# Performance work log

Hardware: AMD Instinct MI355X
Metric: run time of the kernel (lower is better)

The kernel has to match this reference:

```python
import jax, jax.numpy as jnp
import numpy as np

V, H, B, T = 64, 128, 128, 512


def setup_inputs() -> dict:
    key = jax.random.key(0)
    ks = jax.random.split(key, 12)
    s = 0.05
    return {
        "x": jax.random.randint(ks[0], (B, T), 0, V),
        "emb": jax.random.normal(ks[1], (V, H), dtype=jnp.float32) * s,
        "w_ih_f": jax.random.normal(ks[2], (4 * H, H), dtype=jnp.float32) * s,
        "w_hh_f": jax.random.normal(ks[3], (4 * H, H), dtype=jnp.float32) * s,
        "b_ih_f": jax.random.normal(ks[4], (4 * H,), dtype=jnp.float32) * s,
        "b_hh_f": jax.random.normal(ks[5], (4 * H,), dtype=jnp.float32) * s,
        "w_ih_b": jax.random.normal(ks[6], (4 * H, H), dtype=jnp.float32) * s,
        "w_hh_b": jax.random.normal(ks[7], (4 * H, H), dtype=jnp.float32) * s,
        "b_ih_b": jax.random.normal(ks[8], (4 * H,), dtype=jnp.float32) * s,
        "b_hh_b": jax.random.normal(ks[9], (4 * H,), dtype=jnp.float32) * s,
        "fc_w": jax.random.normal(ks[10], (V, 2 * H), dtype=jnp.float32) * s,
        "fc_b": jax.random.normal(ks[11], (V,), dtype=jnp.float32) * s,
    }


def _lstm_scan(xp, w_hh):
    # xp: [T, B, 4H] precomputed input projections (+ biases); w_hh: [4H, H]
    h_dim = w_hh.shape[1]
    b = xp.shape[1]
    h0 = jnp.zeros((b, h_dim), dtype=xp.dtype)
    c0 = jnp.zeros((b, h_dim), dtype=xp.dtype)

    def step(carry, xt):
        h, c = carry
        gates = xt + h @ w_hh.T  # [B, 4H]
        i, f, g, o = jnp.split(gates, 4, axis=-1)  # torch gate order: i, f, g, o
        i = jax.nn.sigmoid(i)
        f = jax.nn.sigmoid(f)
        g = jnp.tanh(g)
        o = jax.nn.sigmoid(o)
        c = f * c + i * g
        h = o * jnp.tanh(c)
        return (h, c), h

    _, hs = jax.lax.scan(step, (h0, c0), xp)
    return hs  # [T, B, H]


def reference(x, emb, w_ih_f, w_hh_f, b_ih_f, b_hh_f,
              w_ih_b, w_hh_b, b_ih_b, b_hh_b, fc_w, fc_b):
    # embedding lookup: [B, T, H]
    e = emb[x]
    # precompute gate input projections for both directions
    xp_f = jnp.einsum('bth,gh->tbg', e, w_ih_f) + (b_ih_f + b_hh_f)  # [T,B,4H]
    xp_b = jnp.einsum('bth,gh->tbg', e, w_ih_b) + (b_ih_b + b_hh_b)
    h_f = _lstm_scan(xp_f, w_hh_f)                    # [T, B, H]
    h_b = _lstm_scan(xp_b[::-1], w_hh_b)[::-1]        # reversed-time dir, flipped back
    out = jnp.concatenate([h_f, h_b], axis=-1)        # [T, B, 2H]
    out = jnp.transpose(out, (1, 0, 2))               # [B, T, 2H]
    return out @ fc_w.T + fc_b                        # [B, T, V]
```

## Files before the change

### kernel.cpp

```cpp
#include <hip/hip_runtime.h>
#include <hip/hip_bf16.h>

#define B_ 128
#define T_ 512
#define H_ 128
#define V_ 64
#define G4_ 512

typedef _Float16 h2_t __attribute__((ext_vector_type(2)));
typedef _Float16 h8_t __attribute__((ext_vector_type(8)));

__device__ __forceinline__ float dot2f(h2_t a, h2_t b, float c) {
#if __has_builtin(__builtin_amdgcn_fdot2)
  return __builtin_amdgcn_fdot2(a, b, c, false);
#else
  return fmaf((float)a[1], (float)b[1], fmaf((float)a[0], (float)b[0], c));
#endif
}

__device__ __forceinline__ float ex2(float x) {
#if __has_builtin(__builtin_amdgcn_exp2f)
  return __builtin_amdgcn_exp2f(x);
#else
  return exp2f(x);
#endif
}

__device__ __forceinline__ float rcpf_(float x) {
#if __has_builtin(__builtin_amdgcn_rcpf)
  return __builtin_amdgcn_rcpf(x);
#else
  return 1.0f / x;
#endif
}

__device__ __forceinline__ float sigm(float x) {
  return rcpf_(1.0f + ex2(-1.4426950408889634f * x));
}
__device__ __forceinline__ float tanh_(float x) {
  float e = ex2(2.8853900817779268f * x);
  return (e - 1.0f) * rcpf_(e + 1.0f);
}

__global__ __launch_bounds__(512) void k_tables(
    const float* __restrict__ emb,
    const float* __restrict__ w_ih_f, const float* __restrict__ b_ih_f,
    const float* __restrict__ b_hh_f,
    const float* __restrict__ w_ih_b, const float* __restrict__ b_ih_b,
    const float* __restrict__ b_hh_b,
    float* __restrict__ Ptab) {
  const int dir = blockIdx.x >> 6;
  const int v = blockIdx.x & 63;
  const int j = threadIdx.x;
  const float* w_ih = dir ? w_ih_b : w_ih_f;
  const float* bi = dir ? b_ih_b : b_ih_f;
  const float* bh = dir ? b_hh_b : b_hh_f;
  const float4* e4 = (const float4*)(emb + v * H_);
  const float4* w4 = (const float4*)(w_ih + j * H_);
  float a0 = 0.f, a1 = 0.f, a2 = 0.f, a3 = 0.f;
#pragma unroll
  for (int q = 0; q < H_ / 4; ++q) {
    float4 e = e4[q];
    float4 w = w4[q];
    a0 = fmaf(e.x, w.x, a0);
    a1 = fmaf(e.y, w.y, a1);
    a2 = fmaf(e.z, w.z, a2);
    a3 = fmaf(e.w, w.w, a3);
  }
  Ptab[dir * (V_ * G4_) + v * G4_ + j] = (a0 + a1) + (a2 + a3) + bi[j] + bh[j];
}

__global__ __launch_bounds__(512, 1) void k_scan(
    const int* __restrict__ x,
    const float* __restrict__ w_hh_f,
    const float* __restrict__ w_hh_b,
    const float* __restrict__ Ptab,
    _Float16* __restrict__ hs) {
  __shared__ __align__(16) float P[V_ * G4_];
  __shared__ float gates[G4_];
  __shared__ __align__(16) h8_t hbuf8[H_ / 8];
  __shared__ int xoff[T_];

  const int tid = threadIdx.x;
  const int b = blockIdx.x >> 1;
  const int dir = blockIdx.x & 1;

  {
    const float4* src = (const float4*)(Ptab + dir * (V_ * G4_));
    float4* dst = (float4*)P;
#pragma unroll
    for (int i = 0; i < (V_ * G4_ / 4) / 512; ++i)
      dst[tid + i * 512] = src[tid + i * 512];
  }
  xoff[tid] = x[(b << 9) + tid] << 9;
  if (tid < H_) ((_Float16*)hbuf8)[tid] = (_Float16)0.f;

  const float* W = (dir ? w_hh_b : w_hh_f) + tid * H_;
  h2_t w2[H_ / 2];
#pragma unroll
  for (int kk = 0; kk < H_ / 2; ++kk) {
    float2 ww = ((const float2*)W)[kk];
    w2[kk] = h2_t{(_Float16)ww.x, (_Float16)ww.y};
  }

  float c_reg = 0.f;
  const int gtype = tid >> 7;
  __syncthreads();

  for (int s = 0; s < T_; ++s) {
    const int t = dir ? (T_ - 1 - s) : s;
    float acc0 = P[xoff[t] + tid];
    float acc1 = 0.f, acc2 = 0.f, acc3 = 0.f;
#pragma unroll
    for (int q = 0; q < H_ / 8; ++q) {
      h8_t hv = hbuf8[q];
      acc0 = dot2f(h2_t{hv[0], hv[1]}, w2[4 * q + 0], acc0);
      acc1 = dot2f(h2_t{hv[2], hv[3]}, w2[4 * q + 1], acc1);
      acc2 = dot2f(h2_t{hv[4], hv[5]}, w2[4 * q + 2], acc2);
      ac3:;
      acc3 = dot2f(h2_t{hv[6], hv[7]}, w2[4 * q + 3], acc3);
    }
    float gv = (acc0 + acc1) + (acc2 + acc3);
    gates[tid] = (gtype == 2) ? tanh_(gv) : sigm(gv);
    __syncthreads();
    if (tid < H_) {
      float gi = gates[tid];
      float gf = gates[H_ + tid];
      float gg = gates[2 * H_ + tid];
      float go = gates[3 * H_ + tid];
      c_reg = fmaf(gf, c_reg, gi * gg);
      float hv = go * tanh_(c_reg);
      ((_Float16*)hbuf8)[tid] = (_Float16)hv;
      hs[(((size_t)(b << 9) + t) << 8) + (dir << 7) + tid] = (_Float16)hv;
    }
    __syncthreads();
  }
}

__global__ __launch_bounds__(256) void k_fc(
    const _Float16* __restrict__ hs,
    const float* __restrict__ fc_w,
    const float* __restrict__ fc_b,
    float* __restrict__ out) {
  __shared__ __align__(16) _Float16 Wl[V_ * 2 * H_];
  __shared__ float bl[V_];
  const int tid = threadIdx.x;
  for (int i = tid; i < V_ * 2 * H_; i += 256) Wl[i] = (_Float16)fc_w[i];
  if (tid < V_) bl[tid] = fc_b[tid];
  __syncthreads();

  const size_t row = (size_t)blockIdx.x * 256 + tid;
  const h8_t* h8 = (const h8_t*)(hs + (row << 8));
  float acc[V_];
#pragma unroll
  for (int v = 0; v < V_; ++v) acc[v] = 0.f;

  for (int ch = 0; ch < 8; ++ch) {
    h8_t hv0 = h8[ch * 4 + 0];
    h8_t hv1 = h8[ch * 4 + 1];
    h8_t hv2 = h8[ch * 4 + 2];
    h8_t hv3 = h8[ch * 4 + 3];
#pragma unroll
    for (int v = 0; v < V_; ++v) {
      const h8_t* w8 = (const h8_t*)(Wl + v * 256 + ch * 32);
      float a = acc[v];
      h8_t wv = w8[0];
      a = dot2f(h2_t{hv0[0], hv0[1]}, h2_t{wv[0], wv[1]}, a);
      a = dot2f(h2_t{hv0[2], hv0[3]}, h2_t{wv[2], wv[3]}, a);
      a = dot2f(h2_t{hv0[4], hv0[5]}, h2_t{wv[4], wv[5]}, a);
      a = dot2f(h2_t{hv0[6], hv0[7]}, h2_t{wv[6], wv[7]}, a);
      wv = w8[1];
      a = dot2f(h2_t{hv1[0], hv1[1]}, h2_t{wv[0], wv[1]}, a);
      a = dot2f(h2_t{hv1[2], hv1[3]}, h2_t{wv[2], wv[3]}, a);
      a = dot2f(h2_t{hv1[4], hv1[5]}, h2_t{wv[4], wv[5]}, a);
      a = dot2f(h2_t{hv1[6], hv1[7]}, h2_t{wv[6], wv[7]}, a);
      wv = w8[2];
      a = dot2f(h2_t{hv2[0], hv2[1]}, h2_t{wv[0], wv[1]}, a);
      a = dot2f(h2_t{hv2[2], hv2[3]}, h2_t{wv[2], wv[3]}, a);
      a = dot2f(h2_t{hv2[4], hv2[5]}, h2_t{wv[4], wv[5]}, a);
      a = dot2f(h2_t{hv2[6], hv2[7]}, h2_t{wv[6], wv[7]}, a);
      wv = w8[3];
      a = dot2f(h2_t{hv3[0], hv3[1]}, h2_t{wv[0], wv[1]}, a);
      a = dot2f(h2_t{hv3[2], hv3[3]}, h2_t{wv[2], wv[3]}, a);
      a = dot2f(h2_t{hv3[4], hv3[5]}, h2_t{wv[4], wv[5]}, a);
      a = dot2f(h2_t{hv3[6], hv3[7]}, h2_t{wv[6], wv[7]}, a);
      acc[v] = a;
    }
  }
  float* orow = out + (row << 6);
#pragma unroll
  for (int v = 0; v < V_; v += 4) {
    float4 o = make_float4(acc[v] + bl[v], acc[v + 1] + bl[v + 1],
                           acc[v + 2] + bl[v + 2], acc[v + 3] + bl[v + 3]);
    *(float4*)(orow + v) = o;
  }
}

extern "C" void kernel_launch(void* const* d_in, const int* in_sizes, int n_in,
                              void* d_out, int out_size, void* d_ws, size_t ws_size,
                              hipStream_t stream) {
  const int* x = (const int*)d_in[0];
  const float* emb = (const float*)d_in[1];
  const float* w_ih_f = (const float*)d_in[2];
  const float* w_hh_f = (const float*)d_in[3];
  const float* b_ih_f = (const float*)d_in[4];
  const float* b_hh_f = (const float*)d_in[5];
  const float* w_ih_b = (const float*)d_in[6];
  const float* w_hh_b = (const float*)d_in[7];
  const float* b_ih_b = (const float*)d_in[8];
  const float* b_hh_b = (const float*)d_in[9];
  const float* fc_w = (const float*)d_in[10];
  const float* fc_b = (const float*)d_in[11];
  float* out = (float*)d_out;

  float* Ptab = (float*)d_ws;
  _Float16* hs = (_Float16*)((char*)d_ws + (size_t)2 * V_ * G4_ * sizeof(float));

  k_tables<<<2 * V_, G4_, 0, stream>>>(emb, w_ih_f, b_ih_f, b_hh_f, w_ih_b,
                                       b_ih_b, b_hh_b, Ptab);
  k_scan<<<B_ * 2, G4_, 0, stream>>>(x, w_hh_f, w_hh_b, Ptab, hs);
  k_fc<<<B_ * T_ / 256, 256, 0, stream>>>(hs, fc_w, fc_b, out);
}
```

Before: 366.7 us.

## Regroup scan lanes so each quad holds one hidden unit's gates, one barrier

```diff
diff --git a/kernel.cpp b/kernel.cpp
--- a/kernel.cpp
+++ b/kernel.cpp
@@ -9,6 +9,7 @@
 
 typedef _Float16 h2_t __attribute__((ext_vector_type(2)));
 typedef _Float16 h8_t __attribute__((ext_vector_type(8)));
+struct h8s { h2_t p[4]; };
 
 __device__ __forceinline__ float dot2f(h2_t a, h2_t b, float c) {
 #if __has_builtin(__builtin_amdgcn_fdot2)
@@ -34,12 +35,27 @@
 #endif
 }
 
-__device__ __forceinline__ float sigm(float x) {
-  return rcpf_(1.0f + ex2(-1.4426950408889634f * x));
-}
-__device__ __forceinline__ float tanh_(float x) {
-  float e = ex2(2.8853900817779268f * x);
-  return (e - 1.0f) * rcpf_(e + 1.0f);
+#define QP_XOR1 0xB1
+#define QP_XOR2 0x4E
+#define QP_BC0 0x00
+#define QP_BC1 0x55
+#define QP_BC2 0xAA
+#define QP_BC3 0xFF
+
+template <int CTRL>
+__device__ __forceinline__ float qperm(float v) {
+#if __has_builtin(__builtin_amdgcn_update_dpp)
+  return __builtin_bit_cast(
+      float, __builtin_amdgcn_update_dpp(0, __builtin_bit_cast(int, v), CTRL,
+                                         0xf, 0xf, true));
+#else
+  int lane = (int)(threadIdx.x & 3);
+  int src;
+  if constexpr (CTRL == QP_XOR1) src = lane ^ 1;
+  else if constexpr (CTRL == QP_XOR2) src = lane ^ 2;
+  else src = CTRL & 3;
+  return __shfl(v, ((int)threadIdx.x & ~3) + src, 64);
+#endif
 }
 
 __global__ __launch_bounds__(512) void k_tables(
@@ -77,13 +93,16 @@
     const float* __restrict__ Ptab,
     _Float16* __restrict__ hs) {
   __shared__ __align__(16) float P[V_ * G4_];
-  __shared__ float gates[G4_];
-  __shared__ __align__(16) h8_t hbuf8[H_ / 8];
   __shared__ int xoff[T_];
+  __shared__ __align__(16) _Float16 hb[2][H_];
 
   const int tid = threadIdx.x;
   const int b = blockIdx.x >> 1;
   const int dir = blockIdx.x & 1;
+  const int l = tid & 63;
+  const int w = tid >> 6;
+  const int g = l & 3;
+  const int k = (w << 4) + (l >> 2);
 
   {
     const float4* src = (const float4*)(Ptab + dir * (V_ * G4_));
@@ -93,47 +112,101 @@
       dst[tid + i * 512] = src[tid + i * 512];
   }
   xoff[tid] = x[(b << 9) + tid] << 9;
-  if (tid < H_) ((_Float16*)hbuf8)[tid] = (_Float16)0.f;
-
-  const float* W = (dir ? w_hh_b : w_hh_f) + tid * H_;
-  h2_t w2[H_ / 2];
-#pragma unroll
-  for (int kk = 0; kk < H_ / 2; ++kk) {
-    float2 ww = ((const float2*)W)[kk];
-    w2[kk] = h2_t{(_Float16)ww.x, (_Float16)ww.y};
-  }
-
-  float c_reg = 0.f;
-  const int gtype = tid >> 7;
+  if (tid < H_) hb[0][tid] = (_Float16)0.f;
+
+  const float* W = dir ? w_hh_b : w_hh_f;
+  h2_t wr[4][16];
+#pragma unroll
+  for (int j = 0; j < 4; ++j) {
+    const float2* wp = (const float2*)(W + (j * H_ + k) * H_ + g * 32);
+#pragma unroll
+    for (int e = 0; e < 16; ++e) {
+      float2 ww = wp[e];
+      wr[j][e] = h2_t{(_Float16)ww.x, (_Float16)ww.y};
+    }
+  }
+
+  const float nm = (g == 2) ? -2.8853900817779268f : -1.4426950408889634f;
+  const float sa = (g == 2) ? 2.f : 1.f;
+  const float sb = (g == 2) ? -1.f : 0.f;
+
+  float c0 = 0.f;
+  _Float16* hsp = hs + ((size_t)(b << 9) << 8) + (dir << 7) + k;
+
   __syncthreads();
 
+  int cur = 0;
   for (int s = 0; s < T_; ++s) {
     const int t = dir ? (T_ - 1 - s) : s;
-    float acc0 = P[xoff[t] + tid];
-    float acc1 = 0.f, acc2 = 0.f, acc3 = 0.f;
-#pragma unroll
-    for (int q = 0; q < H_ / 8; ++q) {
-      h8_t hv = hbuf8[q];
-      acc0 = dot2f(h2_t{hv[0], hv[1]}, w2[4 * q + 0], acc0);
-      acc1 = dot2f(h2_t{hv[2], hv[3]}, w2[4 * q + 1], acc1);
-      acc2 = dot2f(h2_t{hv[4], hv[5]}, w2[4 * q + 2], acc2);
-      ac3:;
-      acc3 = dot2f(h2_t{hv[6], hv[7]}, w2[4 * q + 3], acc3);
-    }
-    float gv = (acc0 + acc1) + (acc2 + acc3);
-    gates[tid] = (gtype == 2) ? tanh_(gv) : sigm(gv);
+    const h8_t* hq8 = (const h8_t*)(&hb[cur][g << 5]);
+    h8s q0 = __builtin_bit_cast(h8s, hq8[0]);
+    h8s q1 = __builtin_bit_cast(h8s, hq8[1]);
+    h8s q2 = __builtin_bit_cast(h8s, hq8[2]);
+    h8s q3 = __builtin_bit_cast(h8s, hq8[3]);
+    float pv = P[xoff[t] + (g << 7) + k];
+
+    float a0 = 0.f, a1 = 0.f, a2 = 0.f, a3 = 0.f;
+#pragma unroll
+    for (int e = 0; e < 4; ++e) {
+      a0 = dot2f(q0.p[e], wr[0][e], a0);
+      a1 = dot2f(q0.p[e], wr[1][e], a1);
+      a2 = dot2f(q0.p[e], wr[2][e], a2);
+      a3 = dot2f(q0.p[e], wr[3][e], a3);
+    }
+#pragma unroll
+    for (int e = 0; e < 4; ++e) {
+      a0 = dot2f(q1.p[e], wr[0][4 + e], a0);
+      a1 = dot2f(q1.p[e], wr[1][4 + e], a1);
+      a2 = dot2f(q1.p[e], wr[2][4 + e], a2);
+      a3 = dot2f(q1.p[e], wr[3][4 + e], a3);
+    }
+#pragma unroll
+    for (int e = 0; e < 4; ++e) {
+      a0 = dot2f(q2.p[e], wr[0][8 + e], a0);
+      a1 = dot2f(q2.p[e], wr[1][8 + e], a1);
+      a2 = dot2f(q2.p[e], wr[2][8 + e], a2);
+      a3 = dot2f(q2.p[e], wr[3][8 + e], a3);
+    }
+#pragma unroll
+    for (int e = 0; e < 4; ++e) {
+      a0 = dot2f(q3.p[e], wr[0][12 + e], a0);
+      a1 = dot2f(q3.p[e], wr[1][12 + e], a1);
+      a2 = dot2f(q3.p[e], wr[2][12 + e], a2);
+      a3 = dot2f(q3.p[e], wr[3][12 + e], a3);
+    }
+
+    float s0 = a0 + qperm<QP_XOR1>(a0);
+    float s1 = a1 + qperm<QP_XOR1>(a1);
+    float s2 = a2 + qperm<QP_XOR1>(a2);
+    float s3 = a3 + qperm<QP_XOR1>(a3);
+    float A = (g & 1) ? s1 : s0;
+    float Bv = (g & 1) ? s3 : s2;
+    float A2 = A + qperm<QP_XOR2>(A);
+    float B2 = Bv + qperm<QP_XOR2>(Bv);
+    float gv = ((g & 2) ? B2 : A2) + pv;
+
+    float e0 = ex2(nm * gv);
+    float r0 = rcpf_(1.f + e0);
+    float y = fmaf(sa, r0, sb);
+
+    float yi = qperm<QP_BC0>(y);
+    float yf = qperm<QP_BC1>(y);
+    float yg = qperm<QP_BC2>(y);
+    float yo = qperm<QP_BC3>(y);
+
+    c0 = fmaf(yf, c0, yi * yg);
+    float ec = ex2(-2.8853900817779268f * c0);
+    float rc = rcpf_(1.f + ec);
+    float tc = fmaf(2.f, rc, -1.f);
+    float ht = yo * tc;
+
+    if (g == 0) {
+      _Float16 hh = (_Float16)ht;
+      hb[cur ^ 1][k] = hh;
+      hsp[(size_t)t << 8] = hh;
+    }
     __syncthreads();
-    if (tid < H_) {
-      float gi = gates[tid];
-      float gf = gates[H_ + tid];
-      float gg = gates[2 * H_ + tid];
-      float go = gates[3 * H_ + tid];
-      c_reg = fmaf(gf, c_reg, gi * gg);
-      float hv = go * tanh_(c_reg);
-      ((_Float16*)hbuf8)[tid] = (_Float16)hv;
-      hs[(((size_t)(b << 9) + t) << 8) + (dir << 7) + tid] = (_Float16)hv;
-    }
-    __syncthreads();
+    cur ^= 1;
   }
 }
 
@@ -156,34 +229,34 @@
   for (int v = 0; v < V_; ++v) acc[v] = 0.f;
 
   for (int ch = 0; ch < 8; ++ch) {
-    h8_t hv0 = h8[ch * 4 + 0];
-    h8_t hv1 = h8[ch * 4 + 1];
-    h8_t hv2 = h8[ch * 4 + 2];
-    h8_t hv3 = h8[ch * 4 + 3];
+    h8s hv0 = __builtin_bit_cast(h8s, h8[ch * 4 + 0]);
+    h8s hv1 = __builtin_bit_cast(h8s, h8[ch * 4 + 1]);
+    h8s hv2 = __builtin_bit_cast(h8s, h8[ch * 4 + 2]);
+    h8s hv3 = __builtin_bit_cast(h8s, h8[ch * 4 + 3]);
 #pragma unroll
     for (int v = 0; v < V_; ++v) {
       const h8_t* w8 = (const h8_t*)(Wl + v * 256 + ch * 32);
       float a = acc[v];
-      h8_t wv = w8[0];
-      a = dot2f(h2_t{hv0[0], hv0[1]}, h2_t{wv[0], wv[1]}, a);
-      a = dot2f(h2_t{hv0[2], hv0[3]}, h2_t{wv[2], wv[3]}, a);
-      a = dot2f(h2_t{hv0[4], hv0[5]}, h2_t{wv[4], wv[5]}, a);
-      a = dot2f(h2_t{hv0[6], hv0[7]}, h2_t{wv[6], wv[7]}, a);
-      wv = w8[1];
-      a = dot2f(h2_t{hv1[0], hv1[1]}, h2_t{wv[0], wv[1]}, a);
-      a = dot2f(h2_t{hv1[2], hv1[3]}, h2_t{wv[2], wv[3]}, a);
-      a = dot2f(h2_t{hv1[4], hv1[5]}, h2_t{wv[4], wv[5]}, a);
-      a = dot2f(h2_t{hv1[6], hv1[7]}, h2_t{wv[6], wv[7]}, a);
-      wv = w8[2];
-      a = dot2f(h2_t{hv2[0], hv2[1]}, h2_t{wv[0], wv[1]}, a);
-      a = dot2f(h2_t{hv2[2], hv2[3]}, h2_t{wv[2], wv[3]}, a);
-      a = dot2f(h2_t{hv2[4], hv2[5]}, h2_t{wv[4], wv[5]}, a);
-      a = dot2f(h2_t{hv2[6], hv2[7]}, h2_t{wv[6], wv[7]}, a);
-      wv = w8[3];
-      a = dot2f(h2_t{hv3[0], hv3[1]}, h2_t{wv[0], wv[1]}, a);
-      a = dot2f(h2_t{hv3[2], hv3[3]}, h2_t{wv[2], wv[3]}, a);
-      a = dot2f(h2_t{hv3[4], hv3[5]}, h2_t{wv[4], wv[5]}, a);
-      a = dot2f(h2_t{hv3[6], hv3[7]}, h2_t{wv[6], wv[7]}, a);
+      h8s wv = __builtin_bit_cast(h8s, w8[0]);
+      a = dot2f(hv0.p[0], wv.p[0], a);
+      a = dot2f(hv0.p[1], wv.p[1], a);
+      a = dot2f(hv0.p[2], wv.p[2], a);
+      a = dot2f(hv0.p[3], wv.p[3], a);
+      wv = __builtin_bit_cast(h8s, w8[1]);
+      a = dot2f(hv1.p[0], wv.p[0], a);
+      a = dot2f(hv1.p[1], wv.p[1], a);
+      a = dot2f(hv1.p[2], wv.p[2], a);
+      a = dot2f(hv1.p[3], wv.p[3], a);
+      wv = __builtin_bit_cast(h8s, w8[2]);
+      a = dot2f(hv2.p[0], wv.p[0], a);
+      a = dot2f(hv2.p[1], wv.p[1], a);
+      a = dot2f(hv2.p[2], wv.p[2], a);
+      a = dot2f(hv2.p[3], wv.p[3], a);
+      wv = __builtin_bit_cast(h8s, w8[3]);
+      a = dot2f(hv3.p[0], wv.p[0], a);
+      a = dot2f(hv3.p[1], wv.p[1], a);
+      a = dot2f(hv3.p[2], wv.p[2], a);
+      a = dot2f(hv3.p[3], wv.p[3], a);
       acc[v] = a;
     }
   }
```

New measurement: 342.8 us. 1.07x faster.
